# Performance work log

Measured on AMD Instinct MI355X. Metric: run time of the kernel, lower is better.

Reference implementation:

```python
import jax, jax.numpy as jnp
import numpy as np

B, INPUT_DIM, HIDDEN, NUM_ASSETS, NUM_HEADS = 16384, 256, 1024, 512, 4


def setup_inputs() -> dict:
    key = jax.random.key(0)
    ks = jax.random.split(key, 8)
    x = jax.random.normal(ks[0], (B, INPUT_DIM), dtype=jnp.float32)
    # last column holds the regime index as a float in {0,1,2,3}
    regime = jax.random.randint(ks[1], (B,), 0, NUM_HEADS)
    x = x.at[:, -1].set(regime.astype(jnp.float32))
    s = 0.02
    W1 = jax.random.normal(ks[2], (INPUT_DIM, HIDDEN), dtype=jnp.float32) * s
    b1 = jnp.zeros((HIDDEN,), dtype=jnp.float32)
    W2 = jax.random.normal(ks[3], (HIDDEN, HIDDEN), dtype=jnp.float32) * s
    b2 = jnp.zeros((HIDDEN,), dtype=jnp.float32)
    # 4 regime heads, stacked: [E, HIDDEN, NUM_ASSETS]
    Wh = jax.random.normal(ks[4], (NUM_HEADS, HIDDEN, NUM_ASSETS), dtype=jnp.float32) * s
    bh = jnp.zeros((NUM_HEADS, NUM_ASSETS), dtype=jnp.float32)
    return {"x": x, "W1": W1, "b1": b1, "W2": W2, "b2": b2, "Wh": Wh, "bh": bh}


def reference(x, W1, b1, W2, b2, Wh, bh):
    # regime id from last feature column (hard routing, non-differentiable)
    regime = x[:, -1].astype(jnp.int32)                      # [B]
    # dense MLP feature extractor
    h = jax.nn.relu(x @ W1 + b1)                             # [B, HIDDEN]
    h = jax.nn.relu(h @ W2 + b2)                             # [B, HIDDEN]
    # compute all 4 heads, then one-hot select (rows with regime outside
    # 0..3 get zeros, matching the torch pre-zeroed scatter semantics)
    out_all = jnp.einsum('bh,ehm->bem', h, Wh) + bh[None]    # [B, 4, NUM_ASSETS]
    onehot = (regime[:, None] == jnp.arange(NUM_HEADS)).astype(h.dtype)  # [B, 4]
    out = jnp.einsum('be,bem->bm', onehot, out_all)          # [B, NUM_ASSETS]
    alpha = jax.nn.softplus(out) + 1.0
    return alpha
```

## Files before the change

kernel.cpp:

```cpp
#include <hip/hip_runtime.h>
#include <hip/hip_bf16.h>
#include <stdint.h>

#define BSZ   16384
#define INDIM 256
#define HID   1024
#define NA    512
#define NE    4
#define BM 128
#define BN 128
#define BK 32
#define PADM (BSZ + NE * BM)

typedef __hip_bfloat16 bf16;
typedef __attribute__((ext_vector_type(8))) short    short8;
typedef __attribute__((ext_vector_type(4))) float    f32x4;
typedef __attribute__((ext_vector_type(8))) unsigned short u16x8;

__device__ __forceinline__ void gload16(const void* g, void* l) {
  __builtin_amdgcn_global_load_lds(
      (__attribute__((address_space(1))) void*)g,
      (__attribute__((address_space(3))) void*)l, 16, 0, 0);
}

__global__ void k_zero(int* cnt, int* cursor) {
  if (threadIdx.x < NE) { cnt[threadIdx.x] = 0; cursor[threadIdx.x] = 0; }
}

__global__ void k_count(const float* __restrict__ x, int* __restrict__ cnt) {
  __shared__ int h[NE];
  const int t = threadIdx.x;
  if (t < NE) h[t] = 0;
  __syncthreads();
  int i = blockIdx.x * blockDim.x + t;
  int r = (int)x[(size_t)i * INDIM + (INDIM - 1)];
  if (r >= 0 && r < NE) atomicAdd(&h[r], 1);
  __syncthreads();
  if (t < NE && h[t] > 0) atomicAdd(&cnt[t], h[t]);
}

__global__ void k_prefix(const int* __restrict__ cnt, int* __restrict__ poff) {
  if (threadIdx.x == 0) {
    int a = 0;
    for (int e = 0; e < NE; ++e) {
      poff[e] = a;
      a += (cnt[e] + BM - 1) / BM * BM;
    }
    poff[NE] = a;
  }
}

__global__ void k_scatter(const float* __restrict__ x, const int* __restrict__ poff,
                          int* __restrict__ cursor, int* __restrict__ sortidx,
                          int* __restrict__ rowid) {
  __shared__ int h[NE], base[NE];
  const int t = threadIdx.x;
  if (t < NE) h[t] = 0;
  __syncthreads();
  int i = blockIdx.x * blockDim.x + t;
  int r = (int)x[(size_t)i * INDIM + (INDIM - 1)];
  int lrank = -1;
  if (r >= 0 && r < NE) lrank = atomicAdd(&h[r], 1);
  __syncthreads();
  if (t < NE) base[t] = (h[t] > 0) ? atomicAdd(&cursor[t], h[t]) : 0;
  __syncthreads();
  if (r >= 0 && r < NE) {
    int p = poff[r] + base[r] + lrank;
    sortidx[i] = p;
    rowid[p] = i;
  }
}

__global__ void k_cast_perm(const float* __restrict__ x, const int* __restrict__ sortidx,
                            bf16* __restrict__ xb) {
  int i = blockIdx.x * blockDim.x + threadIdx.x;
  int row = i >> 5, c8 = (i & 31) * 8;
  int drow = sortidx[row];
  const float4* s = (const float4*)(x + (size_t)row * INDIM + c8);
  float4 a = s[0], b = s[1];
  bf16 t[8];
  t[0] = __float2bfloat16(a.x); t[1] = __float2bfloat16(a.y);
  t[2] = __float2bfloat16(a.z); t[3] = __float2bfloat16(a.w);
  t[4] = __float2bfloat16(b.x); t[5] = __float2bfloat16(b.y);
  t[6] = __float2bfloat16(b.z); t[7] = __float2bfloat16(b.w);
  *(u16x8*)(xb + (size_t)drow * INDIM + c8) = *(u16x8*)t;
}

__global__ void k_transpose(const float* __restrict__ src, bf16* __restrict__ dst,
                            int R, int C) {
  __shared__ float tile[32][33];
  const float* s = src + (size_t)blockIdx.z * R * C;
  bf16* d = dst + (size_t)blockIdx.z * R * C;
  int c0 = blockIdx.x * 32, r0 = blockIdx.y * 32;
  int tx = threadIdx.x, ty = threadIdx.y;
#pragma unroll
  for (int i = 0; i < 32; i += 8)
    tile[ty + i][tx] = s[(size_t)(r0 + ty + i) * C + c0 + tx];
  __syncthreads();
#pragma unroll
  for (int i = 0; i < 32; i += 8)
    d[(size_t)(c0 + ty + i) * R + r0 + tx] = __float2bfloat16(tile[tx][ty + i]);
}

#define STAGE(pa, pb, sa, sb, KK)                                       \
  { _Pragma("unroll")                                                   \
    for (int s = 0; s < 2; ++s) {                                       \
      gload16((pa) + (size_t)s * 64 * (KK), (char*)(sa) + s * 4096 + w * 1024); \
      gload16((pb) + (size_t)s * 64 * (KK), (char*)(sb) + s * 4096 + w * 1024); \
    } }

#define COMPUTE(sa, sb)                                                 \
  { short8 af[4], bfr[4];                                               \
    _Pragma("unroll")                                                   \
    for (int m = 0; m < 4; ++m)                                         \
      af[m] = *(const short8*)&(sa)[(wr * 64 + m * 16 + lr) * BK + lk]; \
    _Pragma("unroll")                                                   \
    for (int n = 0; n < 4; ++n)                                         \
      bfr[n] = *(const short8*)&(sb)[(wc * 64 + n * 16 + lr) * BK + lk];\
    _Pragma("unroll")                                                   \
    for (int m = 0; m < 4; ++m)                                         \
      _Pragma("unroll")                                                 \
      for (int n = 0; n < 4; ++n)                                       \
        acc[m][n] = __builtin_amdgcn_mfma_f32_16x16x32_bf16(af[m], bfr[n], acc[m][n], 0, 0, 0); }

#define KLOOP(pa, pb, KK)                                               \
  STAGE(pa, pb, sA[0], sB[0], KK); (pa) += BK; (pb) += BK;              \
  _Pragma("unroll 2")                                                   \
  for (int kt = 0; kt < (KK) / BK; ++kt) {                              \
    if (kt + 1 < (KK) / BK) {                                           \
      STAGE(pa, pb, sA[(kt + 1) & 1], sB[(kt + 1) & 1], KK);            \
      (pa) += BK; (pb) += BK;                                           \
      asm volatile("s_waitcnt vmcnt(4)" ::: "memory");                  \
    } else {                                                            \
      asm volatile("s_waitcnt vmcnt(0)" ::: "memory");                  \
    }                                                                   \
    __builtin_amdgcn_sched_barrier(0);                                  \
    __builtin_amdgcn_s_barrier();                                       \
    COMPUTE(sA[kt & 1], sB[kt & 1]);                                    \
    __builtin_amdgcn_s_barrier();                                       \
  }

template <int K>
__global__ __launch_bounds__(256) void k_gemm_relu(
    const bf16* __restrict__ A, const bf16* __restrict__ Bt,
    const float* __restrict__ bias, bf16* __restrict__ Out, int N) {
  __shared__ bf16 sA[2][BM * BK];
  __shared__ bf16 sB[2][BN * BK];
  const int t = threadIdx.x, w = t >> 6, l = t & 63;
  const int wr = w >> 1, wc = w & 1;
  const int bm0 = blockIdx.y * BM, bn0 = blockIdx.x * BN;
  const int lr = l & 15, lk = (l >> 4) * 8;
  f32x4 acc[4][4] = {};

  const bf16* pA = A + (size_t)(bm0 + (t >> 2)) * K + (t & 3) * 8;
  const bf16* pB = Bt + (size_t)(bn0 + (t >> 2)) * K + (t & 3) * 8;
  KLOOP(pA, pB, K)

#pragma unroll
  for (int m = 0; m < 4; ++m) {
#pragma unroll
    for (int n = 0; n < 4; ++n) {
      int col = bn0 + wc * 64 + n * 16 + lr;
      float bv = bias[col];
#pragma unroll
      for (int r = 0; r < 4; ++r) {
        int row = bm0 + wr * 64 + m * 16 + (l >> 4) * 4 + r;
        float v = acc[m][n][r] + bv;
        v = v > 0.f ? v : 0.f;
        Out[(size_t)row * N + col] = __float2bfloat16(v);
      }
    }
  }
}

__global__ __launch_bounds__(256) void k_gemm_head(
    const bf16* __restrict__ H,
    const bf16* __restrict__ Wht,
    const float* __restrict__ bh,
    const int* __restrict__ poff,
    const int* __restrict__ cnt,
    const int* __restrict__ rowid,
    float* __restrict__ Out) {
  const int mb0 = blockIdx.y * BM;
  if (mb0 >= poff[NE]) return;
  int e = 0;
#pragma unroll
  for (int k = 1; k < NE; ++k) if (mb0 >= poff[k]) e = k;
  const int pend = poff[e] + cnt[e];

  const int t = threadIdx.x, w = t >> 6, l = t & 63;
  const int wr = w >> 1, wc = w & 1;
  const int bn0 = blockIdx.x * BN;
  const int lr = l & 15, lk = (l >> 4) * 8;
  const bf16* Wt = Wht + (size_t)e * NA * HID;

  __shared__ bf16 sA[2][BM * BK];
  __shared__ bf16 sB[2][BN * BK];
  f32x4 acc[4][4] = {};

  const bf16* pA = H + (size_t)(mb0 + (t >> 2)) * HID + (t & 3) * 8;
  const bf16* pB = Wt + (size_t)(bn0 + (t >> 2)) * HID + (t & 3) * 8;
  KLOOP(pA, pB, HID)

#pragma unroll
  for (int m = 0; m < 4; ++m) {
#pragma unroll
    for (int r = 0; r < 4; ++r) {
      int ps = mb0 + wr * 64 + m * 16 + (l >> 4) * 4 + r;
      if (ps < pend) {
        int row = rowid[ps];
#pragma unroll
        for (int n = 0; n < 4; ++n) {
          int col = bn0 + wc * 64 + n * 16 + lr;
          float v = acc[m][n][r] + bh[e * NA + col];
          float sp = (v > 20.f) ? v : log1pf(expf(v));
          Out[(size_t)row * NA + col] = sp + 1.f;
        }
      }
    }
  }
}

extern "C" void kernel_launch(void* const* d_in, const int* in_sizes, int n_in,
                              void* d_out, int out_size, void* d_ws, size_t ws_size,
                              hipStream_t stream) {
  const float* x  = (const float*)d_in[0];
  const float* W1 = (const float*)d_in[1];
  const float* b1 = (const float*)d_in[2];
  const float* W2 = (const float*)d_in[3];
  const float* b2 = (const float*)d_in[4];
  const float* Wh = (const float*)d_in[5];
  const float* bh = (const float*)d_in[6];
  float* out = (float*)d_out;

  char* p = (char*)d_ws;
  bf16* xb  = (bf16*)p; p += (size_t)PADM * INDIM * 2;
  bf16* w1t = (bf16*)p; p += (size_t)HID * INDIM * 2;
  bf16* w2t = (bf16*)p; p += (size_t)HID * HID * 2;
  bf16* wht = (bf16*)p; p += (size_t)NE * NA * HID * 2;
  bf16* h1b = (bf16*)p; p += (size_t)PADM * HID * 2;
  bf16* h2b = (bf16*)p; p += (size_t)PADM * HID * 2;
  int* sortidx = (int*)p; p += (size_t)BSZ * 4;
  int* rowid   = (int*)p; p += (size_t)PADM * 4;
  int* cnt    = (int*)p; p += 256;
  int* poff   = (int*)p; p += 256;
  int* cursor = (int*)p; p += 256;

  const int MB = PADM / BM;

  k_zero<<<1, 64, 0, stream>>>(cnt, cursor);
  k_count<<<BSZ / 256, 256, 0, stream>>>(x, cnt);
  k_prefix<<<1, 64, 0, stream>>>(cnt, poff);
  k_scatter<<<BSZ / 256, 256, 0, stream>>>(x, poff, cursor, sortidx, rowid);

  k_cast_perm<<<BSZ * (INDIM / 8) / 256, 256, 0, stream>>>(x, sortidx, xb);
  k_transpose<<<dim3(HID / 32, INDIM / 32, 1), dim3(32, 8), 0, stream>>>(W1, w1t, INDIM, HID);
  k_transpose<<<dim3(HID / 32, HID / 32, 1), dim3(32, 8), 0, stream>>>(W2, w2t, HID, HID);
  k_transpose<<<dim3(NA / 32, HID / 32, NE), dim3(32, 8), 0, stream>>>(Wh, wht, HID, NA);

  k_gemm_relu<INDIM><<<dim3(HID / BN, MB), 256, 0, stream>>>(xb, w1t, b1, h1b, HID);
  k_gemm_relu<HID><<<dim3(HID / BN, MB), 256, 0, stream>>>(h1b, w2t, b2, h2b, HID);
  k_gemm_head<<<dim3(NA / BN, MB), 256, 0, stream>>>(h2b, wht, bh, poff, cnt, rowid, out);
}
```

Measured before the change: 264.8 us.

## Triple-buffer LDS in GEMM k-loop with interleaved loads and MFMA priority

Replaces the double-buffered LDS k-loop with a three-stage rotating buffer, so global loads run two tiles ahead and only one barrier is needed per k step. Global loads for the next-next tile are split between two MFMA halves, and s_setprio raises wave priority around the MFMA bursts. This aims to hide global-load latency and cut barrier stalls. In exchange it uses 48KB of LDS per block, which can lower occupancy, and the hand-placed waitcnt values must stay correct for the load counts.

```diff
diff --git a/kernel.cpp b/kernel.cpp
--- a/kernel.cpp
+++ b/kernel.cpp
@@ -102,59 +102,91 @@
     d[(size_t)(c0 + ty + i) * R + r0 + tx] = __float2bfloat16(tile[tx][ty + i]);
 }
 
-#define STAGE(pa, pb, sa, sb, KK)                                       \
-  { _Pragma("unroll")                                                   \
-    for (int s = 0; s < 2; ++s) {                                       \
-      gload16((pa) + (size_t)s * 64 * (KK), (char*)(sa) + s * 4096 + w * 1024); \
-      gload16((pb) + (size_t)s * 64 * (KK), (char*)(sb) + s * 4096 + w * 1024); \
-    } }
-
-#define COMPUTE(sa, sb)                                                 \
-  { short8 af[4], bfr[4];                                               \
-    _Pragma("unroll")                                                   \
-    for (int m = 0; m < 4; ++m)                                         \
-      af[m] = *(const short8*)&(sa)[(wr * 64 + m * 16 + lr) * BK + lk]; \
-    _Pragma("unroll")                                                   \
-    for (int n = 0; n < 4; ++n)                                         \
-      bfr[n] = *(const short8*)&(sb)[(wc * 64 + n * 16 + lr) * BK + lk];\
-    _Pragma("unroll")                                                   \
-    for (int m = 0; m < 4; ++m)                                         \
-      _Pragma("unroll")                                                 \
-      for (int n = 0; n < 4; ++n)                                       \
-        acc[m][n] = __builtin_amdgcn_mfma_f32_16x16x32_bf16(af[m], bfr[n], acc[m][n], 0, 0, 0); }
-
-#define KLOOP(pa, pb, KK)                                               \
-  STAGE(pa, pb, sA[0], sB[0], KK); (pa) += BK; (pb) += BK;              \
-  _Pragma("unroll 2")                                                   \
-  for (int kt = 0; kt < (KK) / BK; ++kt) {                              \
-    if (kt + 1 < (KK) / BK) {                                           \
-      STAGE(pa, pb, sA[(kt + 1) & 1], sB[(kt + 1) & 1], KK);            \
-      (pa) += BK; (pb) += BK;                                           \
-      asm volatile("s_waitcnt vmcnt(4)" ::: "memory");                  \
-    } else {                                                            \
-      asm volatile("s_waitcnt vmcnt(0)" ::: "memory");                  \
-    }                                                                   \
-    __builtin_amdgcn_sched_barrier(0);                                  \
-    __builtin_amdgcn_s_barrier();                                       \
-    COMPUTE(sA[kt & 1], sB[kt & 1]);                                    \
-    __builtin_amdgcn_s_barrier();                                       \
+
+#define AFRAG(cur, m) (*(const short8*)((cur) + (wr * 64 + (m)*16 + lr) * 64 + (l >> 4) * 16))
+#define BFRAG(cur, n) (*(const short8*)((cur) + 8192 + (wc * 64 + (n)*16 + lr) * 64 + (l >> 4) * 16))
+
+#define STAGE_KT(pa, pb, dst, KK)                                   \
+  { gload16((pa), (dst) + w * 1024);                                \
+    gload16((pa) + (size_t)64 * (KK), (dst) + 4096 + w * 1024);     \
+    gload16((pb), (dst) + 8192 + w * 1024);                         \
+    gload16((pb) + (size_t)64 * (KK), (dst) + 12288 + w * 1024); }
+
+#define KLOOP3(pa, pb, KK)                                                     \
+  {                                                                            \
+    char* cur = ldsbuf;                                                        \
+    char* nxt = ldsbuf + 16384;                                                \
+    char* stg = ldsbuf + 32768;                                                \
+    STAGE_KT(pa, pb, cur, KK); (pa) += BK; (pb) += BK;                         \
+    STAGE_KT(pa, pb, nxt, KK); (pa) += BK; (pb) += BK;                         \
+    asm volatile("s_waitcnt vmcnt(4)" ::: "memory");                           \
+    __builtin_amdgcn_s_barrier();                                              \
+    const int NT = (KK) / BK;                                                  \
+    for (int kt = 0; kt < NT; ++kt) {                                          \
+      const bool more = (kt + 2 < NT);                                         \
+                         \
+      short8 a0 = AFRAG(cur, 0), a1 = AFRAG(cur, 1);                           \
+      short8 b0 = BFRAG(cur, 0), b1 = BFRAG(cur, 1);                           \
+      short8 b2 = BFRAG(cur, 2), b3 = BFRAG(cur, 3);                           \
+      if (more) {                                                              \
+        gload16((pa), stg + w * 1024);                                         \
+        gload16((pa) + (size_t)64 * (KK), stg + 4096 + w * 1024);              \
+      }                                                                        \
+      asm volatile("s_waitcnt lgkmcnt(0)" ::: "memory");                       \
+      __builtin_amdgcn_sched_barrier(0);                                       \
+      __builtin_amdgcn_s_setprio(1);                                           \
+      acc[0][0] = __builtin_amdgcn_mfma_f32_16x16x32_bf16(a0, b0, acc[0][0], 0, 0, 0); \
+      acc[0][1] = __builtin_amdgcn_mfma_f32_16x16x32_bf16(a0, b1, acc[0][1], 0, 0, 0); \
+      acc[0][2] = __builtin_amdgcn_mfma_f32_16x16x32_bf16(a0, b2, acc[0][2], 0, 0, 0); \
+      acc[0][3] = __builtin_amdgcn_mfma_f32_16x16x32_bf16(a0, b3, acc[0][3], 0, 0, 0); \
+      acc[1][0] = __builtin_amdgcn_mfma_f32_16x16x32_bf16(a1, b0, acc[1][0], 0, 0, 0); \
+      acc[1][1] = __builtin_amdgcn_mfma_f32_16x16x32_bf16(a1, b1, acc[1][1], 0, 0, 0); \
+      acc[1][2] = __builtin_amdgcn_mfma_f32_16x16x32_bf16(a1, b2, acc[1][2], 0, 0, 0); \
+      acc[1][3] = __builtin_amdgcn_mfma_f32_16x16x32_bf16(a1, b3, acc[1][3], 0, 0, 0); \
+      __builtin_amdgcn_s_setprio(0);                                           \
+                                   \
+      short8 a2 = AFRAG(cur, 2), a3 = AFRAG(cur, 3);                           \
+      if (more) {                                                              \
+        gload16((pb), stg + 8192 + w * 1024);                                  \
+        gload16((pb) + (size_t)64 * (KK), stg + 12288 + w * 1024);             \
+        (pa) += BK; (pb) += BK;                                                \
+      }                                                                        \
+      asm volatile("s_waitcnt lgkmcnt(0)" ::: "memory");                       \
+      __builtin_amdgcn_sched_barrier(0);                                       \
+      __builtin_amdgcn_s_setprio(1);                                           \
+      acc[2][0] = __builtin_amdgcn_mfma_f32_16x16x32_bf16(a2, b0, acc[2][0], 0, 0, 0); \
+      acc[2][1] = __builtin_amdgcn_mfma_f32_16x16x32_bf16(a2, b1, acc[2][1], 0, 0, 0); \
+      acc[2][2] = __builtin_amdgcn_mfma_f32_16x16x32_bf16(a2, b2, acc[2][2], 0, 0, 0); \
+      acc[2][3] = __builtin_amdgcn_mfma_f32_16x16x32_bf16(a2, b3, acc[2][3], 0, 0, 0); \
+      acc[3][0] = __builtin_amdgcn_mfma_f32_16x16x32_bf16(a3, b0, acc[3][0], 0, 0, 0); \
+      acc[3][1] = __builtin_amdgcn_mfma_f32_16x16x32_bf16(a3, b1, acc[3][1], 0, 0, 0); \
+      acc[3][2] = __builtin_amdgcn_mfma_f32_16x16x32_bf16(a3, b2, acc[3][2], 0, 0, 0); \
+      acc[3][3] = __builtin_amdgcn_mfma_f32_16x16x32_bf16(a3, b3, acc[3][3], 0, 0, 0); \
+      __builtin_amdgcn_s_setprio(0);                                           \
+      \
+      if (kt + 1 < NT) {                                                       \
+        if (more) { asm volatile("s_waitcnt vmcnt(4)" ::: "memory"); }         \
+        else      { asm volatile("s_waitcnt vmcnt(0)" ::: "memory"); }         \
+        __builtin_amdgcn_s_barrier();                                          \
+      }                                                                        \
+      char* tmp = cur; cur = nxt; nxt = stg; stg = tmp;                        \
+    }                                                                          \
   }
 
 template <int K>
 __global__ __launch_bounds__(256) void k_gemm_relu(
     const bf16* __restrict__ A, const bf16* __restrict__ Bt,
     const float* __restrict__ bias, bf16* __restrict__ Out, int N) {
-  __shared__ bf16 sA[2][BM * BK];
-  __shared__ bf16 sB[2][BN * BK];
+  __shared__ char ldsbuf[49152];
   const int t = threadIdx.x, w = t >> 6, l = t & 63;
   const int wr = w >> 1, wc = w & 1;
   const int bm0 = blockIdx.y * BM, bn0 = blockIdx.x * BN;
-  const int lr = l & 15, lk = (l >> 4) * 8;
+  const int lr = l & 15;
   f32x4 acc[4][4] = {};
 
   const bf16* pA = A + (size_t)(bm0 + (t >> 2)) * K + (t & 3) * 8;
   const bf16* pB = Bt + (size_t)(bn0 + (t >> 2)) * K + (t & 3) * 8;
-  KLOOP(pA, pB, K)
+  KLOOP3(pA, pB, K)
 
 #pragma unroll
   for (int m = 0; m < 4; ++m) {
@@ -188,19 +220,17 @@
   for (int k = 1; k < NE; ++k) if (mb0 >= poff[k]) e = k;
   const int pend = poff[e] + cnt[e];
 
+  __shared__ char ldsbuf[49152];
   const int t = threadIdx.x, w = t >> 6, l = t & 63;
   const int wr = w >> 1, wc = w & 1;
   const int bn0 = blockIdx.x * BN;
-  const int lr = l & 15, lk = (l >> 4) * 8;
+  const int lr = l & 15;
   const bf16* Wt = Wht + (size_t)e * NA * HID;
-
-  __shared__ bf16 sA[2][BM * BK];
-  __shared__ bf16 sB[2][BN * BK];
   f32x4 acc[4][4] = {};
 
   const bf16* pA = H + (size_t)(mb0 + (t >> 2)) * HID + (t & 3) * 8;
   const bf16* pB = Wt + (size_t)(bn0 + (t >> 2)) * HID + (t & 3) * 8;
-  KLOOP(pA, pB, HID)
+  KLOOP3(pA, pB, HID)
 
 #pragma unroll
   for (int m = 0; m < 4; ++m) {
```

After: 252.8 us. -4.5%, faster.
